# Kernel tuning notes

Hardware: AMD Instinct MI355X
Metric: run time of the kernel (lower is better)

The kernel has to match this reference:

```python
import jax, jax.numpy as jnp
import numpy as np

T = 4096      # tokens (flattened batch*seq)
DIN = 2048    # input hidden dim
DQ = 2048     # q output dim
DKV = 2048    # per-head-group kv output dim (== DQ here, MHA)
NA = 4        # number of adapters (LoRA/delta models)
R = 16        # lora rank per q/k/v


def setup_inputs() -> dict:
    key = jax.random.key(0)
    ks = jax.random.split(key, 8)
    def rn(k, shape, scale):
        return jax.random.normal(k, shape, dtype=jnp.float32) * scale
    return {
        "x": rn(ks[0], (T, DIN), 1.0),
        "W_base": rn(ks[1], (DQ + 2 * DKV, DIN), DIN ** -0.5),
        "A_buffer_qkv": rn(ks[2], (NA, DIN, 3 * R), DIN ** -0.5),
        "B_buffer_q": rn(ks[3], (NA, R, DQ), R ** -0.5),
        "B_buffer_kv": rn(ks[4], (NA, R, 2 * DKV), R ** -0.5),
        "DeltaW_q": rn(ks[5], (NA, DIN, DQ), DIN ** -0.5),
        "DeltaW_kv": rn(ks[6], (NA, DIN, 2 * DKV), DIN ** -0.5),
        "weight_indices": jax.random.randint(ks[7], (T,), 0, NA, dtype=jnp.int32),
    }


def _ldmm(indices, x, A, B, D):
    """Per-token adapter-indexed (LoRA + dense delta) matmul.
    indices: [T] int, x: [T, din], A: [na, din, r], B: [na, r, dout], D: [na, din, dout].
    out[t] = (x[t] @ A[a]) @ B[a] + x[t] @ D[a]  with a = indices[t].
    Implemented as masked GEMMs over the small fixed adapter set.
    """
    na = A.shape[0]
    out = jnp.zeros((x.shape[0], B.shape[2]), dtype=x.dtype)
    for a in range(na):  # small fixed loop over adapters
        xa = jnp.where((indices == a)[:, None], x, jnp.zeros((), x.dtype))
        out = out + (xa @ A[a]) @ B[a] + xa @ D[a]
    return out


def reference(x, W_base, A_buffer_qkv, B_buffer_q, B_buffer_kv,
              DeltaW_q, DeltaW_kv, weight_indices):
    # base QKV projection (ColumnParallelLinear, no bias): [T, dq + 2*dkv]
    base = x @ W_base.T
    rank = A_buffer_qkv.shape[2] // 3
    b_dim_q = B_buffer_q.shape[2]
    b_dim_kv = B_buffer_kv.shape[2] // 2
    d_dim_kv = DeltaW_kv.shape[2] // 2
    for i in range(3):  # q, k, v slices
        if i == 0:
            o = _ldmm(weight_indices, x,
                      A_buffer_qkv[:, :, :rank], B_buffer_q, DeltaW_q)
            base = base.at[:, :b_dim_q].add(o)
        else:
            o = _ldmm(weight_indices, x,
                      A_buffer_qkv[:, :, i * rank:(i + 1) * rank],
                      B_buffer_kv[:, :, (i - 1) * b_dim_kv:i * b_dim_kv],
                      DeltaW_kv[:, :, (i - 1) * d_dim_kv:i * d_dim_kv])
            base = base.at[:, i * b_dim_kv:(i + 1) * b_dim_kv].add(o)
    return base
```

## Files before the change

### kernel.cpp

```cpp
#include <hip/hip_runtime.h>
#include <stdint.h>

#define T_TOK 4096
#define DIN   2048
#define DQ    2048
#define DKV   2048
#define NOUT  (DQ + 2*DKV)
#define NA    4
#define RLORA 16
#define BM    256
#define BN    256
#define MPAD  (T_TOK + NA*BM)
#define MTILES (MPAD/BM)
#define KX    (DIN + 64)
#define NKT64 (KX/64)
#define KSPLIT 16
#define NTBLK (NOUT/BN)
#define NWG   (MTILES*NTBLK)

typedef unsigned short u16;
typedef __attribute__((ext_vector_type(8))) short short8;
typedef __attribute__((ext_vector_type(8))) u16 u16x8;
typedef __attribute__((ext_vector_type(4))) float f32x4;

__device__ __forceinline__ u16 f2bf(float f) {
  uint32_t u = __float_as_uint(f);
  u = (u + 0x7FFFu + ((u >> 16) & 1u)) >> 16;
  return (u16)u;
}
__device__ __forceinline__ float bf2f(u16 u) {
  return __uint_as_float(((uint32_t)u) << 16);
}

typedef __attribute__((address_space(3))) void lds_void;
typedef __attribute__((address_space(1))) void glb_void;

__device__ __forceinline__ void gl_lds16(const void* g, void* l) {
  __builtin_amdgcn_global_load_lds((const glb_void*)(uintptr_t)g,
                                   (lds_void*)(uint32_t)(uintptr_t)l, 16, 0, 0);
}

__global__ void prep_kernel(const int* __restrict__ widx,
                            int* __restrict__ tok,
                            int* __restrict__ tileAdapter) {
  __shared__ int cnt[256][NA];
  __shared__ int total[NA];
  __shared__ int pad_off[NA];
  const int tid = threadIdx.x;
  const int CH = T_TOK / 256;
  const int base = tid * CH;
  int c[NA] = {0, 0, 0, 0};
  for (int i = 0; i < CH; i++) c[widx[base + i]]++;
  for (int a = 0; a < NA; a++) cnt[tid][a] = c[a];
  __syncthreads();
  if (tid < NA) {
    int s = 0;
    for (int i = 0; i < 256; i++) { int v = cnt[i][tid]; cnt[i][tid] = s; s += v; }
    total[tid] = s;
  }
  __syncthreads();
  if (tid == 0) {
    int off = 0;
    for (int a = 0; a < NA; a++) {
      pad_off[a] = off;
      int ntile = (total[a] + BM - 1) / BM;
      for (int tl = 0; tl < ntile; tl++) tileAdapter[off / BM + tl] = a;
      off += ntile * BM;
    }
    for (int tl = off / BM; tl < MTILES; tl++) tileAdapter[tl] = -1;
  }
  __syncthreads();
  for (int i = tid; i < MPAD; i += 256) tok[i] = -1;
  __syncthreads();
  int myoff[NA];
  for (int a = 0; a < NA; a++) myoff[a] = pad_off[a] + cnt[tid][a];
  for (int i = 0; i < CH; i++) {
    int a = widx[base + i];
    tok[myoff[a]++] = base + i;
  }
}

__global__ void gather_kernel(const float* __restrict__ x,
                              const int* __restrict__ tok,
                              u16* __restrict__ Xg) {
  const int row = blockIdx.x;
  const int t = tok[row];
  const int tid = threadIdx.x;
  u16x8* dst = (u16x8*)(Xg + (size_t)row * KX);
  if (t < 0) {
    u16x8 z = {0, 0, 0, 0, 0, 0, 0, 0};
    dst[tid] = z;
    return;
  }
  const f32x4* src = (const f32x4*)(x + (size_t)t * DIN);
  f32x4 v0 = src[tid * 2];
  f32x4 v1 = src[tid * 2 + 1];
  u16x8 o;
  o[0] = f2bf(v0[0]); o[1] = f2bf(v0[1]); o[2] = f2bf(v0[2]); o[3] = f2bf(v0[3]);
  o[4] = f2bf(v1[0]); o[5] = f2bf(v1[1]); o[6] = f2bf(v1[2]); o[7] = f2bf(v1[3]);
  dst[tid] = o;
}

__global__ __launch_bounds__(256) void xa_partial_kernel(
    const u16* __restrict__ Xg, const float* __restrict__ A_qkv,
    const int* __restrict__ tileAdapter, float* __restrict__ Ppart) {
  const int ks = blockIdx.y;
  const int ad = tileAdapter[blockIdx.x >> 1];
  const int a = ad < 0 ? 0 : ad;
  const int kb = ks * (DIN / KSPLIT);
  const int tid = threadIdx.x;
  const int rg = tid >> 2;
  const int jg = tid & 3;
  const int r0 = blockIdx.x * 128 + rg * 2;
  const int j0 = jg * 12;
  __shared__ float ldsA[64][56];
  float acc[2][12];
  #pragma unroll
  for (int r = 0; r < 2; r++)
    #pragma unroll
    for (int j = 0; j < 12; j++) acc[r][j] = 0.f;

  for (int kc = 0; kc < 2; kc++) {
    const int kbase = kb + kc * 64;
    for (int i = tid; i < 64 * 48; i += 256) {
      int kk = i / 48, j = i - kk * 48;
      ldsA[kk][j] = A_qkv[((size_t)a * DIN + kbase + kk) * (3 * RLORA) + j];
    }
    __syncthreads();
    u16x8 xr[2][8];
    #pragma unroll
    for (int r = 0; r < 2; r++)
      #pragma unroll
      for (int q = 0; q < 8; q++)
        xr[r][q] = *(const u16x8*)(Xg + (size_t)(r0 + r) * KX + kbase + q * 8);
    #pragma unroll
    for (int q = 0; q < 8; q++) {
      #pragma unroll
      for (int e = 0; e < 8; e++) {
        const int kk = q * 8 + e;
        f32x4 a0 = *(const f32x4*)&ldsA[kk][j0];
        f32x4 a1 = *(const f32x4*)&ldsA[kk][j0 + 4];
        f32x4 a2 = *(const f32x4*)&ldsA[kk][j0 + 8];
        float x0 = bf2f(xr[0][q][e]);
        float x1 = bf2f(xr[1][q][e]);
        #pragma unroll
        for (int c = 0; c < 4; c++) {
          acc[0][c]     += x0 * a0[c];  acc[1][c]     += x1 * a0[c];
          acc[0][4 + c] += x0 * a1[c];  acc[1][4 + c] += x1 * a1[c];
          acc[0][8 + c] += x0 * a2[c];  acc[1][8 + c] += x1 * a2[c];
        }
      }
    }
    __syncthreads();
  }
  #pragma unroll
  for (int r = 0; r < 2; r++)
    #pragma unroll
    for (int j = 0; j < 12; j++)
      Ppart[((size_t)ks * MPAD + r0 + r) * 48 + j0 + j] = acc[r][j];
}

__global__ void xa_reduce_kernel(const float* __restrict__ Ppart,
                                 u16* __restrict__ Xg) {
  const int gid = blockIdx.x * 256 + threadIdx.x;
  const int row = gid >> 6, j = gid & 63;
  float s = 0.f;
  if (j < 48) {
    #pragma unroll
    for (int sp = 0; sp < KSPLIT; sp++)
      s += Ppart[((size_t)sp * MPAD + row) * 48 + j];
  }
  Xg[(size_t)row * KX + DIN + j] = f2bf(s);
}

__global__ __launch_bounds__(256) void weff2_kernel(
    const float* __restrict__ W_base,
    const float* __restrict__ DW_q, const float* __restrict__ DW_kv,
    u16* __restrict__ Weff) {
  const int k0 = blockIdx.x * 64;
  const int n0 = blockIdx.y * 64;
  const int tid = threadIdx.x;
  const int k8 = (tid & 7) * 8;
  __shared__ float ldsD[64][65];

  f32x4 wb[2][2];
  #pragma unroll
  for (int h = 0; h < 2; h++) {
    const int nn = h * 32 + (tid >> 3);
    const float* p = W_base + (size_t)(n0 + nn) * DIN + k0 + k8;
    wb[h][0] = *(const f32x4*)p;
    wb[h][1] = *(const f32x4*)(p + 4);
  }

  const int ldD  = (n0 < DQ) ? DQ : 2 * DKV;
  const int ncol = (n0 < DQ) ? n0 : n0 - DQ;

  for (int a = 0; a < NA; a++) {
    const float* Dp = (n0 < DQ)
        ? DW_q  + (size_t)a * DIN * DQ + ncol
        : DW_kv + (size_t)a * DIN * (2 * DKV) + ncol;
    for (int i = tid; i < 64 * 64; i += 256) {
      int kk = i >> 6, nn2 = i & 63;
      ldsD[kk][nn2] = Dp[(size_t)(k0 + kk) * ldD + nn2];
    }
    __syncthreads();
    #pragma unroll
    for (int h = 0; h < 2; h++) {
      const int nn = h * 32 + (tid >> 3);
      u16x8 o;
      #pragma unroll
      for (int j = 0; j < 8; j++)
        o[j] = f2bf(wb[h][j >> 2][j & 3] + ldsD[k8 + j][nn]);
      *(u16x8*)(Weff + ((size_t)a * NOUT + n0 + nn) * KX + k0 + k8) = o;
    }
    __syncthreads();
  }
}

__global__ void wslots_kernel(const float* __restrict__ B_q,
                              const float* __restrict__ B_kv,
                              u16* __restrict__ Weff) {
  const int a = blockIdx.y;
  const int n = blockIdx.x * 256 + threadIdx.x;
  const int seg = n >> 11;
  u16 vals[64];
  #pragma unroll
  for (int j = 0; j < 64; j++) vals[j] = 0;
  if (seg == 0) {
    const float* Bp = B_q + ((size_t)a * RLORA) * DQ + n;
    #pragma unroll
    for (int r = 0; r < RLORA; r++) vals[r] = f2bf(Bp[(size_t)r * DQ]);
  } else if (seg == 1) {
    const float* Bp = B_kv + ((size_t)a * RLORA) * (2 * DKV) + (n - DQ);
    #pragma unroll
    for (int r = 0; r < RLORA; r++) vals[RLORA + r] = f2bf(Bp[(size_t)r * (2 * DKV)]);
  } else {
    const float* Bp = B_kv + ((size_t)a * RLORA) * (2 * DKV) + (n - DQ);
    #pragma unroll
    for (int r = 0; r < RLORA; r++) vals[2 * RLORA + r] = f2bf(Bp[(size_t)r * (2 * DKV)]);
  }
  u16* dst = Weff + ((size_t)a * NOUT + n) * KX + DIN;
  #pragma unroll
  for (int v = 0; v < 8; v++) *(u16x8*)(dst + v * 8) = *(u16x8*)(vals + v * 8);
}

#define BAR      asm volatile("s_barrier" ::: "memory")
#define WAITV(n) asm volatile("s_waitcnt vmcnt(" #n ")" ::: "memory")

#define RD_A(db, mh) { \
  _Pragma("unroll") for (int q = 0; q < 4; ++q) { \
    const char* rp = ldsc + (db)*32768 + (wm*128 + (mh)*64 + q*16 + fr)*128; \
    af[q][0] = *(const short8*)(rp + ck0); \
    af[q][1] = *(const short8*)(rp + ck1); } }

#define RD_B(db, nh, bfv) { \
  _Pragma("unroll") for (int q = 0; q < 2; ++q) { \
    const char* rp = ldsc + 65536 + (db)*32768 + ((nh)*128 + wn*32 + q*16 + fr)*128; \
    bfv[q][0] = *(const short8*)(rp + ck0); \
    bfv[q][1] = *(const short8*)(rp + ck1); } }

#define ST_A(db, mh, t) { \
  gl_lds16(gAsrc + (size_t)((mh)*64)*KX + (size_t)(t)*64, \
           ldsu + (db)*16384 + ((mh)*64*64) + stid); \
  gl_lds16(gAsrc + (size_t)(128 + (mh)*64)*KX + (size_t)(t)*64, \
           ldsu + (db)*16384 + ((128 + (mh)*64)*64) + stid); }

#define ST_B(db, nh, t) { \
  gl_lds16(gBsrc + (size_t)((nh)*32)*KX + (size_t)(t)*64, \
           ldsu + 32768 + (db)*16384 + ((nh)*128*64) + stid); \
  gl_lds16(gBsrc + (size_t)(128 + (nh)*32)*KX + (size_t)(t)*64, \
           ldsu + 32768 + (db)*16384 + (((nh)*128 + 64)*64) + stid); }

#define MM(mh, nh, bfv) { \
  __builtin_amdgcn_s_setprio(1); \
  _Pragma("unroll") for (int q = 0; q < 4; ++q) \
  _Pragma("unroll") for (int r = 0; r < 2; ++r) { \
    acc[(mh)*4+q][(nh)*2+r] = __builtin_amdgcn_mfma_f32_16x16x32_bf16( \
        af[q][0], bfv[r][0], acc[(mh)*4+q][(nh)*2+r], 0, 0, 0); \
    acc[(mh)*4+q][(nh)*2+r] = __builtin_amdgcn_mfma_f32_16x16x32_bf16( \
        af[q][1], bfv[r][1], acc[(mh)*4+q][(nh)*2+r], 0, 0, 0); } \
  __builtin_amdgcn_s_setprio(0); }

#define KT_STD(db, t) { \
  RD_A(db, 0); RD_B(db, 0, bf0); ST_A(1-(db), 1, (t)+1); BAR; MM(0, 0, bf0); BAR; \
  RD_B(db, 1, bf1);              ST_B(1-(db), 0, (t)+1); BAR; MM(0, 1, bf1); BAR; \
  RD_A(db, 1);                   ST_A(db, 0, (t)+2);     BAR; MM(1, 1, bf1); BAR; \
  ST_B(db, 1, (t)+2); WAITV(4);                          BAR; MM(1, 0, bf0); BAR; }

#define KT_T31(db, t) { \
  RD_A(db, 0); RD_B(db, 0, bf0); ST_A(1-(db), 1, (t)+1); BAR; MM(0, 0, bf0); BAR; \
  RD_B(db, 1, bf1);              ST_B(1-(db), 0, (t)+1); BAR; MM(0, 1, bf1); BAR; \
  RD_A(db, 1);                                           BAR; MM(1, 1, bf1); BAR; \
  WAITV(0);                                              BAR; MM(1, 0, bf0); BAR; }

#define KT_LAST(db) { \
  RD_A(db, 0); RD_B(db, 0, bf0); BAR; MM(0, 0, bf0); BAR; \
  RD_B(db, 1, bf1);              BAR; MM(0, 1, bf1); BAR; \
  RD_A(db, 1);                   BAR; MM(1, 1, bf1); BAR; \
                                 BAR; MM(1, 0, bf0); BAR; }

__global__ __launch_bounds__(512, 2) void gemm256_kernel(
    const u16* __restrict__ Xg, const u16* __restrict__ Weff,
    const int* __restrict__ tok, const int* __restrict__ tileAdapter,
    float* __restrict__ out) {
  __shared__ __align__(16) u16 Lds[65536];

  const int bid = blockIdx.x;
  const int wg = (bid & 7) * (NWG / 8) + (bid >> 3);
  const int mt = wg % MTILES, nt = wg / MTILES;
  const int a = tileAdapter[mt];
  if (a < 0) return;
  const int m0 = mt * BM, n0 = nt * BN;

  const int tid = threadIdx.x;
  const int l = tid & 63, w = tid >> 6;
  const int wm = w >> 2, wn = w & 3;
  const int fr = l & 15;
  const int kq = l >> 4;
  const int s7 = l & 7;
  const int ck0 = ((kq ^ s7) << 4);
  const int ck1 = (((4 + kq) ^ s7) << 4);

  const int l64 = tid >> 3;
  const int swc = (tid & 7) ^ (l64 & 7);
  const int stid = tid * 8;
  const u16* gAsrc = Xg + (size_t)(m0 + l64) * KX + swc * 8;
  const int nB = ((l64 >> 5) * 64) + (l64 & 31);
  const u16* gBsrc = Weff + ((size_t)a * NOUT + n0 + nB) * KX + swc * 8;

  u16* ldsu = &Lds[0];
  const char* ldsc = (const char*)ldsu;

  f32x4 acc[8][4];
  #pragma unroll
  for (int i = 0; i < 8; i++)
    #pragma unroll
    for (int j = 0; j < 4; j++) acc[i][j] = (f32x4){0.f, 0.f, 0.f, 0.f};

  short8 af[4][2], bf0[2][2], bf1[2][2];

  ST_A(0, 0, 0); ST_B(0, 0, 0); ST_A(0, 1, 0); ST_B(0, 1, 0);
  ST_A(1, 0, 1); ST_B(1, 1, 1);
  WAITV(4);
  BAR;

  for (int p = 0; p < 15; ++p) {
    const int t0 = 2 * p;
    KT_STD(0, t0);
    KT_STD(1, t0 + 1);
  }
  KT_STD(0, 30);
  KT_T31(1, 31);
  KT_LAST(0);

  #pragma unroll
  for (int mi = 0; mi < 8; ++mi) {
    const int rb = m0 + wm * 128 + mi * 16 + ((l >> 4) << 2);
    int tt[4];
    #pragma unroll
    for (int reg = 0; reg < 4; ++reg) tt[reg] = tok[rb + reg];
    #pragma unroll
    for (int ni = 0; ni < 4; ++ni) {
      const int col = n0 + wn * 64 + ni * 16 + fr;
      #pragma unroll
      for (int reg = 0; reg < 4; ++reg)
        if (tt[reg] >= 0) out[(size_t)tt[reg] * NOUT + col] = acc[mi][ni][reg];
    }
  }
}

__global__ void fallback_kernel(const float* __restrict__ x,
                                const float* __restrict__ W_base,
                                const float* __restrict__ A_qkv,
                                const float* __restrict__ B_q,
                                const float* __restrict__ B_kv,
                                const float* __restrict__ DW_q,
                                const float* __restrict__ DW_kv,
                                const int* __restrict__ widx,
                                float* __restrict__ out) {
  const int t = blockIdx.x;
  const int n = blockIdx.y * 256 + threadIdx.x;
  const int a = widx[t];
  __shared__ float xs[DIN];
  __shared__ float ys[3 * RLORA];
  for (int k = threadIdx.x; k < DIN; k += 256) xs[k] = x[(size_t)t * DIN + k];
  __syncthreads();
  if (threadIdx.x < 3 * RLORA) {
    float s = 0.f;
    const float* Ap = A_qkv + (size_t)a * DIN * (3 * RLORA) + threadIdx.x;
    for (int k = 0; k < DIN; k++) s += xs[k] * Ap[(size_t)k * (3 * RLORA)];
    ys[threadIdx.x] = s;
  }
  __syncthreads();
  const float* dcol; int ldD, roff; const float* bcol; int ldB;
  if (n < DQ) {
    dcol = DW_q + (size_t)a * DIN * DQ + n; ldD = DQ; roff = 0;
    bcol = B_q + (size_t)a * RLORA * DQ + n; ldB = DQ;
  } else {
    dcol = DW_kv + (size_t)a * DIN * (2 * DKV) + (n - DQ); ldD = 2 * DKV;
    roff = (n < 2 * DQ) ? RLORA : 2 * RLORA;
    bcol = B_kv + (size_t)a * RLORA * (2 * DKV) + (n - DQ); ldB = 2 * DKV;
  }
  const float* wrow = W_base + (size_t)n * DIN;
  float acc = 0.f;
  for (int k = 0; k < DIN; k++) acc += xs[k] * (wrow[k] + dcol[(size_t)k * ldD]);
  for (int r = 0; r < RLORA; r++) acc += ys[roff + r] * bcol[(size_t)r * ldB];
  out[(size_t)t * NOUT + n] = acc;
}

extern "C" void kernel_launch(void* const* d_in, const int* in_sizes, int n_in,
                              void* d_out, int out_size, void* d_ws, size_t ws_size,
                              hipStream_t stream) {
  const float* x      = (const float*)d_in[0];
  const float* W_base = (const float*)d_in[1];
  const float* A_qkv  = (const float*)d_in[2];
  const float* B_q    = (const float*)d_in[3];
  const float* B_kv   = (const float*)d_in[4];
  const float* DW_q   = (const float*)d_in[5];
  const float* DW_kv  = (const float*)d_in[6];
  const int*   widx   = (const int*)d_in[7];
  float* out = (float*)d_out;

  const size_t WEFF_BYTES = (size_t)NA * NOUT * KX * sizeof(u16);
  const size_t XG_BYTES   = (size_t)MPAD * KX * sizeof(u16);
  const size_t TOK_BYTES  = (size_t)MPAD * sizeof(int);
  const size_t TILE_BYTES = (size_t)MTILES * sizeof(int);
  const size_t need = WEFF_BYTES + XG_BYTES + TOK_BYTES + TILE_BYTES;

  if (ws_size < need) {
    fallback_kernel<<<dim3(T_TOK, NOUT / 256), 256, 0, stream>>>(
        x, W_base, A_qkv, B_q, B_kv, DW_q, DW_kv, widx, out);
    return;
  }

  char* ws = (char*)d_ws;
  u16* Weff = (u16*)ws;
  u16* Xg   = (u16*)(ws + WEFF_BYTES);
  int* tok  = (int*)(ws + WEFF_BYTES + XG_BYTES);
  int* tileAdapter = tok + MPAD;
  float* Ppart = (float*)ws;

  prep_kernel<<<1, 256, 0, stream>>>(widx, tok, tileAdapter);
  gather_kernel<<<MPAD, 256, 0, stream>>>(x, tok, Xg);
  xa_partial_kernel<<<dim3(MPAD / 128, KSPLIT), 256, 0, stream>>>(
      Xg, A_qkv, tileAdapter, Ppart);
  xa_reduce_kernel<<<MPAD * 64 / 256, 256, 0, stream>>>(Ppart, Xg);
  weff2_kernel<<<dim3(DIN / 64, NOUT / 64), 256, 0, stream>>>(
      W_base, DW_q, DW_kv, Weff);
  wslots_kernel<<<dim3(NOUT / 256, NA), 256, 0, stream>>>(B_q, B_kv, Weff);
  gemm256_kernel<<<dim3(NWG), 512, 0, stream>>>(
      Xg, Weff, tok, tileAdapter, out);
}
```

Baseline: 248.5 us.

## Fold LoRA B-slot packing into weff kernel, prefetch delta tiles, add LDS waitcnt

Merges the wslots kernel into weff2 as an extra column of blocks, which removes one kernel launch. In weff2 the next adapter's DeltaW tile is now prefetched into registers with vectorized f32x4 loads while the current one is staged to LDS, so global latency overlaps with compute. In the GEMM main loop an explicit lgkmcnt(8) wait is placed before the first barrier of each k-step. That wait may change how LDS reads overlap with the MFMA work.

```diff
diff --git a/kernel.cpp b/kernel.cpp
--- a/kernel.cpp
+++ b/kernel.cpp
@@ -176,10 +176,40 @@
 __global__ __launch_bounds__(256) void weff2_kernel(
     const float* __restrict__ W_base,
     const float* __restrict__ DW_q, const float* __restrict__ DW_kv,
+    const float* __restrict__ B_q,  const float* __restrict__ B_kv,
     u16* __restrict__ Weff) {
+  const int tid = threadIdx.x;
+  const int n0 = blockIdx.y * 64;
+
+  if (blockIdx.x == DIN / 64) {
+    const int a = tid >> 6;
+    const int n = n0 + (tid & 63);
+    const int seg = n >> 11;
+    u16 vals[64];
+    #pragma unroll
+    for (int j = 0; j < 64; j++) vals[j] = 0;
+    if (seg == 0) {
+      const float* Bp = B_q + ((size_t)a * RLORA) * DQ + n;
+      #pragma unroll
+      for (int r = 0; r < RLORA; r++) vals[r] = f2bf(Bp[(size_t)r * DQ]);
+    } else if (seg == 1) {
+      const float* Bp = B_kv + ((size_t)a * RLORA) * (2 * DKV) + (n - DQ);
+      #pragma unroll
+      for (int r = 0; r < RLORA; r++)
+        vals[RLORA + r] = f2bf(Bp[(size_t)r * (2 * DKV)]);
+    } else {
+      const float* Bp = B_kv + ((size_t)a * RLORA) * (2 * DKV) + (n - DQ);
+      #pragma unroll
+      for (int r = 0; r < RLORA; r++)
+        vals[2 * RLORA + r] = f2bf(Bp[(size_t)r * (2 * DKV)]);
+    }
+    u16* dst = Weff + ((size_t)a * NOUT + n) * KX + DIN;
+    #pragma unroll
+    for (int v = 0; v < 8; v++) *(u16x8*)(dst + v * 8) = *(u16x8*)(vals + v * 8);
+    return;
+  }
+
   const int k0 = blockIdx.x * 64;
-  const int n0 = blockIdx.y * 64;
-  const int tid = threadIdx.x;
   const int k8 = (tid & 7) * 8;
   __shared__ float ldsD[64][65];
 
@@ -194,14 +224,28 @@
 
   const int ldD  = (n0 < DQ) ? DQ : 2 * DKV;
   const int ncol = (n0 < DQ) ? n0 : n0 - DQ;
+  const float* Dbase = (n0 < DQ) ? (DW_q + ncol) : (DW_kv + ncol);
+  const size_t Dstride = (n0 < DQ) ? (size_t)DIN * DQ : (size_t)DIN * (2 * DKV);
+
+  const int lkk  = tid >> 4;
+  const int lnn4 = (tid & 15) * 4;
+
+  f32x4 v4[4];
+  #pragma unroll
+  for (int j = 0; j < 4; j++)
+    v4[j] = *(const f32x4*)(Dbase + (size_t)(k0 + lkk + 16 * j) * ldD + lnn4);
 
   for (int a = 0; a < NA; a++) {
-    const float* Dp = (n0 < DQ)
-        ? DW_q  + (size_t)a * DIN * DQ + ncol
-        : DW_kv + (size_t)a * DIN * (2 * DKV) + ncol;
-    for (int i = tid; i < 64 * 64; i += 256) {
-      int kk = i >> 6, nn2 = i & 63;
-      ldsD[kk][nn2] = Dp[(size_t)(k0 + kk) * ldD + nn2];
+    #pragma unroll
+    for (int j = 0; j < 4; j++)
+      #pragma unroll
+      for (int c = 0; c < 4; c++)
+        ldsD[lkk + 16 * j][lnn4 + c] = v4[j][c];
+    if (a < NA - 1) {
+      const float* Dp = Dbase + (size_t)(a + 1) * Dstride;
+      #pragma unroll
+      for (int j = 0; j < 4; j++)
+        v4[j] = *(const f32x4*)(Dp + (size_t)(k0 + lkk + 16 * j) * ldD + lnn4);
     }
     __syncthreads();
     #pragma unroll
@@ -217,35 +261,9 @@
   }
 }
 
-__global__ void wslots_kernel(const float* __restrict__ B_q,
-                              const float* __restrict__ B_kv,
-                              u16* __restrict__ Weff) {
-  const int a = blockIdx.y;
-  const int n = blockIdx.x * 256 + threadIdx.x;
-  const int seg = n >> 11;
-  u16 vals[64];
-  #pragma unroll
-  for (int j = 0; j < 64; j++) vals[j] = 0;
-  if (seg == 0) {
-    const float* Bp = B_q + ((size_t)a * RLORA) * DQ + n;
-    #pragma unroll
-    for (int r = 0; r < RLORA; r++) vals[r] = f2bf(Bp[(size_t)r * DQ]);
-  } else if (seg == 1) {
-    const float* Bp = B_kv + ((size_t)a * RLORA) * (2 * DKV) + (n - DQ);
-    #pragma unroll
-    for (int r = 0; r < RLORA; r++) vals[RLORA + r] = f2bf(Bp[(size_t)r * (2 * DKV)]);
-  } else {
-    const float* Bp = B_kv + ((size_t)a * RLORA) * (2 * DKV) + (n - DQ);
-    #pragma unroll
-    for (int r = 0; r < RLORA; r++) vals[2 * RLORA + r] = f2bf(Bp[(size_t)r * (2 * DKV)]);
-  }
-  u16* dst = Weff + ((size_t)a * NOUT + n) * KX + DIN;
-  #pragma unroll
-  for (int v = 0; v < 8; v++) *(u16x8*)(dst + v * 8) = *(u16x8*)(vals + v * 8);
-}
-
 #define BAR      asm volatile("s_barrier" ::: "memory")
 #define WAITV(n) asm volatile("s_waitcnt vmcnt(" #n ")" ::: "memory")
+#define LGKM8    asm volatile("s_waitcnt lgkmcnt(8)" ::: "memory")
 
 #define RD_A(db, mh) { \
   _Pragma("unroll") for (int q = 0; q < 4; ++q) { \
@@ -282,19 +300,19 @@
   __builtin_amdgcn_s_setprio(0); }
 
 #define KT_STD(db, t) { \
-  RD_A(db, 0); RD_B(db, 0, bf0); ST_A(1-(db), 1, (t)+1); BAR; MM(0, 0, bf0); BAR; \
+  RD_A(db, 0); RD_B(db, 0, bf0); ST_A(1-(db), 1, (t)+1); LGKM8; BAR; MM(0, 0, bf0); BAR; \
   RD_B(db, 1, bf1);              ST_B(1-(db), 0, (t)+1); BAR; MM(0, 1, bf1); BAR; \
   RD_A(db, 1);                   ST_A(db, 0, (t)+2);     BAR; MM(1, 1, bf1); BAR; \
   ST_B(db, 1, (t)+2); WAITV(4);                          BAR; MM(1, 0, bf0); BAR; }
 
 #define KT_T31(db, t) { \
-  RD_A(db, 0); RD_B(db, 0, bf0); ST_A(1-(db), 1, (t)+1); BAR; MM(0, 0, bf0); BAR; \
+  RD_A(db, 0); RD_B(db, 0, bf0); ST_A(1-(db), 1, (t)+1); LGKM8; BAR; MM(0, 0, bf0); BAR; \
   RD_B(db, 1, bf1);              ST_B(1-(db), 0, (t)+1); BAR; MM(0, 1, bf1); BAR; \
   RD_A(db, 1);                                           BAR; MM(1, 1, bf1); BAR; \
   WAITV(0);                                              BAR; MM(1, 0, bf0); BAR; }
 
 #define KT_LAST(db) { \
-  RD_A(db, 0); RD_B(db, 0, bf0); BAR; MM(0, 0, bf0); BAR; \
+  RD_A(db, 0); RD_B(db, 0, bf0); LGKM8; BAR; MM(0, 0, bf0); BAR; \
   RD_B(db, 1, bf1);              BAR; MM(0, 1, bf1); BAR; \
   RD_A(db, 1);                   BAR; MM(1, 1, bf1); BAR; \
                                  BAR; MM(1, 0, bf0); BAR; }
@@ -445,9 +463,8 @@
   xa_partial_kernel<<<dim3(MPAD / 128, KSPLIT), 256, 0, stream>>>(
       Xg, A_qkv, tileAdapter, Ppart);
   xa_reduce_kernel<<<MPAD * 64 / 256, 256, 0, stream>>>(Ppart, Xg);
-  weff2_kernel<<<dim3(DIN / 64, NOUT / 64), 256, 0, stream>>>(
-      W_base, DW_q, DW_kv, Weff);
-  wslots_kernel<<<dim3(NOUT / 256, NA), 256, 0, stream>>>(B_q, B_kv, Weff);
+  weff2_kernel<<<dim3(DIN / 64 + 1, NOUT / 64), 256, 0, stream>>>(
+      W_base, DW_q, DW_kv, B_q, B_kv, Weff);
   gemm256_kernel<<<dim3(NWG), 512, 0, stream>>>(
       Xg, Weff, tok, tileAdapter, out);
 }
```

Result: no change. 244.9 us (-1.5%).
